# Kernel tuning notes

Hardware: AMD Instinct MI355X
Metric: run time of the kernel (lower is better)

Reference implementation:

```python
import jax, jax.numpy as jnp
import numpy as np
import math

B, T, C_IN = 4, 2048, 1024
HIDDEN, HEADS = 1024, 8
HEAD_DIM = HIDDEN // HEADS
OUT_DIM = 1024
EPS = 1e-8


def setup_inputs() -> dict:
    key = jax.random.key(0)
    ks = jax.random.split(key, 12)
    s_in = 1.0 / math.sqrt(C_IN)
    s_h = 1.0 / math.sqrt(HIDDEN)
    x = jax.random.normal(ks[0], (B, T, C_IN), dtype=jnp.float32)
    # causal keep-mask (True = keep), broadcast over batch
    attn_mask = jnp.broadcast_to(jnp.tril(jnp.ones((T, T), dtype=bool)), (B, T, T))
    Wu = jax.random.normal(ks[1], (HIDDEN, C_IN), dtype=jnp.float32) * s_in
    bu = jnp.zeros((HIDDEN,), dtype=jnp.float32)
    Wv = jax.random.normal(ks[2], (HIDDEN, C_IN), dtype=jnp.float32) * s_in
    bv = jnp.zeros((HIDDEN,), dtype=jnp.float32)
    Wq = jax.random.normal(ks[3], (HIDDEN, C_IN), dtype=jnp.float32) * s_in
    bq = jnp.zeros((HIDDEN,), dtype=jnp.float32)
    Wk = jax.random.normal(ks[4], (HIDDEN, C_IN), dtype=jnp.float32) * s_in
    bk = jnp.zeros((HIDDEN,), dtype=jnp.float32)
    Wf = jax.random.normal(ks[5], (OUT_DIM, HIDDEN), dtype=jnp.float32) * s_h
    bf = jnp.zeros((OUT_DIM,), dtype=jnp.float32)
    g_norm = jnp.ones((HIDDEN,), dtype=jnp.float32)
    return {"x": x, "attn_mask": attn_mask, "Wu": Wu, "bu": bu, "Wv": Wv,
            "bv": bv, "Wq": Wq, "bq": bq, "Wk": Wk, "bk": bk,
            "Wf": Wf, "bf": bf, "g_norm": g_norm}


def _heads(t):  # (B,T,HIDDEN) -> (B,H,T,D)
    b, s, _ = t.shape
    return t.reshape(b, s, HEADS, HEAD_DIM).transpose(0, 2, 1, 3)


def reference(x, attn_mask, Wu, bu, Wv, bv, Wq, bq, Wk, bk, Wf, bf, g_norm):
    silu = jax.nn.silu
    U = silu(x @ Wu.T + bu)
    V = silu(x @ Wv.T + bv)
    Q = silu(x @ Wq.T + bq)
    K = silu(x @ Wk.T + bk)
    Qh, Kh, Vh = _heads(Q), _heads(K), _heads(V)
    scale = 1.0 / math.sqrt(HEAD_DIM)
    logits = jnp.einsum('bhtd,bhsd->bhts', Qh, Kh) * scale
    A = jnp.maximum(silu(logits), 0.0)
    A = jnp.where(attn_mask[:, None, :, :], A, 0.0)
    denom = A.sum(axis=-1, keepdims=True)
    A = jnp.where(denom > 1e-12, A / (denom + EPS), 0.0)
    AVh = jnp.einsum('bhts,bhsd->bhtd', A, Vh)
    AV = AVh.transpose(0, 2, 1, 3).reshape(x.shape[0], x.shape[1], HIDDEN)
    # RMSNorm (torch nn.RMSNorm default eps = dtype eps)
    rms_eps = jnp.finfo(AV.dtype).eps
    AV_norm = AV * jax.lax.rsqrt(jnp.mean(AV * AV, axis=-1, keepdims=True) + rms_eps) * g_norm
    UV = AV_norm * U
    return UV @ Wf.T + bf
```

## Files before the change

kernel.cpp:

```cpp
#include <hip/hip_runtime.h>
#include <hip/hip_bf16.h>
#include <stdint.h>

#define Tlen  2048
#define M_TOK 8192

typedef __attribute__((ext_vector_type(8))) __bf16 bf16x8;
typedef __attribute__((ext_vector_type(4))) float  f32x4;
typedef unsigned short u16;
typedef unsigned int   u32;
typedef unsigned long long u64;

__device__ __forceinline__ float b2f(u16 u) {
  union { float f; u32 i; } v; v.i = ((u32)u) << 16; return v.f;
}
__device__ __forceinline__ u16 f2b(float f) {
  u32 x = __float_as_uint(f);
  return (u16)((x + 0x7FFFu + ((x >> 16) & 1u)) >> 16);
}
__device__ __forceinline__ u32 f2b2(float lo, float hi) {
  __hip_bfloat162 h = __float22bfloat162_rn(float2{lo, hi});
  return *reinterpret_cast<u32*>(&h);
}
__device__ __forceinline__ bf16x8 ld8(const u16* p) {
  return *reinterpret_cast<const bf16x8*>(p);
}
__device__ __forceinline__ bool probe_bf16(const void* g) {
  return *(const u32*)g == 0x3F803F80u;
}
__device__ __forceinline__ void stage8(u16* dst, const void* src, size_t eidx, bool isbf) {
  if (isbf) {
    *(uint4*)dst = *(const uint4*)((const u16*)src + eidx);
  } else {
    const float* f = (const float*)src + eidx;
    float4 a = *(const float4*)f;
    float4 b = *(const float4*)(f + 4);
    u32 t[4] = { f2b2(a.x, a.y), f2b2(a.z, a.w), f2b2(b.x, b.y), f2b2(b.z, b.w) };
    *(uint4*)dst = *(uint4*)t;
  }
}
__device__ __forceinline__ void gl_lds16(const void* g, void* l) {
  __builtin_amdgcn_global_load_lds(
      (const __attribute__((address_space(1))) u32*)g,
      (__attribute__((address_space(3))) u32*)l, 16, 0, 0);
}
__device__ __forceinline__ int swz128(int r, int c) {
  return r * 128 + ((((c >> 3) ^ (r & 15))) << 3) + (c & 7);
}

__global__ __launch_bounds__(256) void prep1(
    const void* __restrict__ x,
    const void* __restrict__ Wu, const void* __restrict__ Wv,
    const void* __restrict__ Wq, const void* __restrict__ Wk,
    const void* __restrict__ bu, const void* __restrict__ bv,
    const void* __restrict__ bq, const void* __restrict__ bk,
    u16* __restrict__ xb, u16* __restrict__ Wcat, u16* __restrict__ bcat,
    const void* __restrict__ gprobe)
{
  const bool isbf = probe_bf16(gprobe);
  long i = (long)blockIdx.x * 256 + threadIdx.x;
  if (i < 1048576) { stage8(&xb[i * 8], x, (size_t)i * 8, isbf); return; }
  i -= 1048576;
  if (i < 524288) {
    int w = (int)(i >> 17); long e = i & 131071;
    const void* s = (w == 0) ? Wu : (w == 1) ? Wv : (w == 2) ? Wq : Wk;
    stage8(&Wcat[((size_t)w << 20) + e * 8], s, (size_t)e * 8, isbf); return;
  }
  i -= 524288;
  if (i < 512) {
    int w = (int)(i >> 7); int e = (int)(i & 127);
    const void* s = (w == 0) ? bu : (w == 1) ? bv : (w == 2) ? bq : bk;
    stage8(&bcat[w * 1024 + e * 8], s, (size_t)e * 8, isbf);
  }
}

__global__ __launch_bounds__(256) void prep2(
    const void* __restrict__ Wf, const void* __restrict__ bf_,
    u16* __restrict__ Wfb, u16* __restrict__ bfb,
    const void* __restrict__ gprobe)
{
  const bool isbf = probe_bf16(gprobe);
  long i = (long)blockIdx.x * 256 + threadIdx.x;
  if (i < 131072) { stage8(&Wfb[i * 8], Wf, (size_t)i * 8, isbf); return; }
  i -= 131072;
  if (i < 128) stage8(&bfb[i * 8], bf_, (size_t)i * 8, isbf);
}

__global__ __launch_bounds__(256) void gemm_proj(
    const u16* __restrict__ X,
    const u16* __restrict__ W,
    const u16* __restrict__ bias,
    u16* __restrict__ U, u16* __restrict__ Vt,
    u16* __restrict__ Qb, u16* __restrict__ Kb)
{
  __shared__ u16 SMEM[16384];
  u16* Xs = SMEM;
  u16* Ws = SMEM + 8192;
  const int tid  = threadIdx.x;
  const int lane = tid & 63;
  const int wave = tid >> 6;
  const int l15  = lane & 15;
  const int quad = lane >> 4;
  const int wr   = wave & 1;
  const int wc   = wave >> 1;
  const int m0 = blockIdx.y * 128;
  const int n0 = blockIdx.x * 128;

  const int ro = lane >> 3;
  const int ch = lane & 7;
  const int cc = ch ^ ro;

  f32x4 acc[4][4] = {};

  for (int k0 = 0; k0 < 1024; k0 += 64) {
    __syncthreads();
#pragma unroll
    for (int j = 0; j < 4; j++) {
      int r0 = wave * 32 + j * 8;
      gl_lds16(X + (size_t)(m0 + r0 + ro) * 1024 + k0 + cc * 8, &Xs[r0 * 64]);
      gl_lds16(W + (size_t)(n0 + r0 + ro) * 1024 + k0 + cc * 8, &Ws[r0 * 64]);
    }
    __syncthreads();

#pragma unroll
    for (int kk = 0; kk < 64; kk += 32) {
      bf16x8 a[4], b[4];
      const int g = (kk >> 3) + quad;
      const int lch = (g ^ (l15 & 7)) << 3;
#pragma unroll
      for (int mt = 0; mt < 4; mt++)
        a[mt] = ld8(&Xs[(wr * 64 + mt * 16 + l15) * 64 + lch]);
#pragma unroll
      for (int nt = 0; nt < 4; nt++)
        b[nt] = ld8(&Ws[(wc * 64 + nt * 16 + l15) * 64 + lch]);
#pragma unroll
      for (int mt = 0; mt < 4; mt++)
#pragma unroll
        for (int nt = 0; nt < 4; nt++)
          acc[mt][nt] = __builtin_amdgcn_mfma_f32_16x16x32_bf16(a[mt], b[nt], acc[mt][nt], 0, 0, 0);
    }
  }

  const int grp = blockIdx.x >> 3;

  if (grp != 1) {
    u16* dst = (grp == 0) ? U : (grp == 2) ? Qb : Kb;
    const float postmul = (grp == 3) ? 0.08838834764831845f : 1.0f;
#pragma unroll
    for (int nt = 0; nt < 4; nt++) {
      int ng = n0 + wc * 64 + nt * 16 + l15;
      float bv = b2f(bias[ng]);
      int ncol = ng & 1023;
#pragma unroll
      for (int mt = 0; mt < 4; mt++) {
#pragma unroll
        for (int r = 0; r < 4; r++) {
          int m = m0 + wr * 64 + mt * 16 + quad * 4 + r;
          float v = acc[mt][nt][r] + bv;
          v = v * __builtin_amdgcn_rcpf(1.0f + __expf(-v));
          dst[(size_t)m * 1024 + ncol] = f2b(v * postmul);
        }
      }
    }
    return;
  }

  u16* Ls = SMEM;
  __syncthreads();
#pragma unroll
  for (int nt = 0; nt < 4; nt++) {
    int ng = n0 + wc * 64 + nt * 16 + l15;
    float bv = b2f(bias[ng]);
    int nl = wc * 64 + nt * 16 + l15;
#pragma unroll
    for (int mt = 0; mt < 4; mt++) {
      float vv[4];
#pragma unroll
      for (int r = 0; r < 4; r++) {
        float v = acc[mt][nt][r] + bv;
        vv[r] = v * __builtin_amdgcn_rcpf(1.0f + __expf(-v));
      }
      int ml = wr * 64 + mt * 16 + quad * 4;
      u64 pk = (u64)f2b2(vv[0], vv[1]) | ((u64)f2b2(vv[2], vv[3]) << 32);
      *(u64*)&Ls[swz128(nl, ml)] = pk;
    }
  }
  __syncthreads();

  const int rr = tid & 127;
  const int c0 = tid >> 7;
  const int bh = (blockIdx.y >> 4) * 8 + (blockIdx.x & 7);
  const int t0 = (blockIdx.y & 15) * 128;
#pragma unroll
  for (int p = 0; p < 8; p++) {
    int chunk = c0 + p * 2;
    uint4 vv = *(const uint4*)&Ls[swz128(rr, chunk * 8)];
    *(uint4*)&Vt[((size_t)bh * 128 + rr) * 2048 + t0 + chunk * 8] = vv;
  }
}

__global__ __launch_bounds__(256) void gemm_final(
    const u16* __restrict__ X,
    const u16* __restrict__ W,
    const u16* __restrict__ bias,
    float* __restrict__ O)
{
  __shared__ u16 Xs[128 * 64];
  __shared__ u16 Ws[64 * 64];
  const int tid  = threadIdx.x;
  const int lane = tid & 63;
  const int wave = tid >> 6;
  const int l15  = lane & 15;
  const int quad = lane >> 4;
  const int m0 = blockIdx.y * 128;
  const int n0 = blockIdx.x * 64;

  const int ro = lane >> 3;
  const int ch = lane & 7;
  const int cc = ch ^ ro;

  f32x4 acc[2][4] = {};

  for (int k0 = 0; k0 < 1024; k0 += 64) {
    __syncthreads();
#pragma unroll
    for (int j = 0; j < 4; j++) {
      int r0 = wave * 32 + j * 8;
      gl_lds16(X + (size_t)(m0 + r0 + ro) * 1024 + k0 + cc * 8, &Xs[r0 * 64]);
    }
#pragma unroll
    for (int j = 0; j < 2; j++) {
      int r0 = wave * 16 + j * 8;
      gl_lds16(W + (size_t)(n0 + r0 + ro) * 1024 + k0 + cc * 8, &Ws[r0 * 64]);
    }
    __syncthreads();

#pragma unroll
    for (int kk = 0; kk < 64; kk += 32) {
      bf16x8 a[2], b[4];
      const int g = (kk >> 3) + quad;
      const int lch = (g ^ (l15 & 7)) << 3;
#pragma unroll
      for (int mt = 0; mt < 2; mt++)
        a[mt] = ld8(&Xs[(wave * 32 + mt * 16 + l15) * 64 + lch]);
#pragma unroll
      for (int nt = 0; nt < 4; nt++)
        b[nt] = ld8(&Ws[(nt * 16 + l15) * 64 + lch]);
#pragma unroll
      for (int mt = 0; mt < 2; mt++)
#pragma unroll
        for (int nt = 0; nt < 4; nt++)
          acc[mt][nt] = __builtin_amdgcn_mfma_f32_16x16x32_bf16(a[mt], b[nt], acc[mt][nt], 0, 0, 0);
    }
  }

#pragma unroll
  for (int nt = 0; nt < 4; nt++) {
    int n = n0 + nt * 16 + l15;
    float bv = b2f(bias[n]);
#pragma unroll
    for (int mt = 0; mt < 2; mt++)
#pragma unroll
      for (int r = 0; r < 4; r++) {
        int m = m0 + wave * 32 + mt * 16 + quad * 4 + r;
        O[(size_t)m * 1024 + n] = acc[mt][nt][r] + bv;
      }
  }
}

__global__ __launch_bounds__(256, 4) void attn_kernel(
    const u16* __restrict__ Q,
    const u16* __restrict__ K,
    const u16* __restrict__ Vt,
    u16* __restrict__ AV)
{
  __shared__ u16 Ks[64 * 128];
  __shared__ u16 Vts[128 * 64];
  u16* As = Ks;

  const int tid  = threadIdx.x;
  const int lane = tid & 63;
  const int wave = tid >> 6;
  const int l15  = lane & 15;
  const int quad = lane >> 4;
  const int qt = 31 - (blockIdx.x >> 5);
  const int bh = blockIdx.x & 31;
  const int q0 = qt * 64;
  const size_t rowbase = (size_t)(bh >> 3) * Tlen;
  const int cbase = (bh & 7) * 128;
  const size_t vbase = (size_t)bh * 128 * 2048;
  const int mrow = wave * 16;

  bf16x8 bq[4];
#pragma unroll
  for (int kk = 0; kk < 4; kk++)
    bq[kk] = ld8(&Q[(rowbase + q0 + mrow + l15) * 1024 + cbase + kk * 32 + quad * 8]);

  f32x4 avacc[8] = {};
  float denom = 0.f;
  const int t_abs = q0 + mrow + l15;

  for (int s0 = 0; s0 <= q0; s0 += 64) {
    __syncthreads();
    {
      const int ro16 = lane >> 4, ch16 = lane & 15;
#pragma unroll
      for (int j = 0; j < 4; j++) {
        int r0 = wave * 16 + j * 4;
        int cc = ch16 ^ ((r0 + ro16) & 15);
        gl_lds16(&K[(rowbase + s0 + r0 + ro16) * 1024 + cbase + cc * 8], &Ks[r0 * 128]);
      }
      const int ro8 = lane >> 3, ch8 = lane & 7;
#pragma unroll
      for (int j = 0; j < 4; j++) {
        int d0 = wave * 32 + j * 8;
        int cc = ch8 ^ ((d0 + ro8) & 7);
        gl_lds16(&Vt[vbase + (size_t)(d0 + ro8) * 2048 + s0 + cc * 8], &Vts[d0 * 64]);
      }
    }
    __syncthreads();

    f32x4 sacc[4] = {};
#pragma unroll
    for (int kk = 0; kk < 4; kk++) {
      bf16x8 a[4];
      const int lch = (((kk * 4) + quad) ^ l15) << 3;
#pragma unroll
      for (int nt = 0; nt < 4; nt++)
        a[nt] = ld8(&Ks[(nt * 16 + l15) * 128 + lch]);
#pragma unroll
      for (int nt = 0; nt < 4; nt++)
        sacc[nt] = __builtin_amdgcn_mfma_f32_16x16x32_bf16(a[nt], bq[kk], sacc[nt], 0, 0, 0);
    }
    __syncthreads();

    const bool maskneed = (s0 + 63 > q0 + mrow);
    float rs = 0.f;
#pragma unroll
    for (int nt = 0; nt < 4; nt++) {
      float aa[4];
#pragma unroll
      for (int r = 0; r < 4; r++) {
        int s_abs = s0 + nt * 16 + quad * 4 + r;
        float z = sacc[nt][r];
        float a = fmaxf(z, 0.f) * __builtin_amdgcn_rcpf(1.0f + __expf(-z));
        if (maskneed && (s_abs > t_abs)) a = 0.0f;
        rs += a;
        aa[r] = a;
      }
      u64 pk = (u64)f2b2(aa[0], aa[1]) | ((u64)f2b2(aa[2], aa[3]) << 32);
      *(u64*)&As[(mrow + l15) * 72 + nt * 16 + quad * 4] = pk;
    }
    rs += __shfl_xor(rs, 16);
    rs += __shfl_xor(rs, 32);
    denom += rs;

#pragma unroll
    for (int kk = 0; kk < 2; kk++) {
      bf16x8 a, b[8];
      const int lch8 = (((kk * 4) + quad) ^ (l15 & 7)) << 3;
      a = ld8(&As[(mrow + l15) * 72 + kk * 32 + quad * 8]);
#pragma unroll
      for (int dt = 0; dt < 8; dt++)
        b[dt] = ld8(&Vts[(dt * 16 + l15) * 64 + lch8]);
#pragma unroll
      for (int dt = 0; dt < 8; dt++)
        avacc[dt] = __builtin_amdgcn_mfma_f32_16x16x32_bf16(a, b[dt], avacc[dt], 0, 0, 0);
    }
  }

  __syncthreads();
  u16* Ls = Ks;
#pragma unroll
  for (int r = 0; r < 4; r++) {
    float dn = __shfl(denom, (lane & 48) | (quad * 4 + r));
    float sc = (dn > 1e-12f) ? __builtin_amdgcn_rcpf(dn + 1e-8f) : 0.0f;
    int rl = mrow + quad * 4 + r;
#pragma unroll
    for (int dt = 0; dt < 8; dt++)
      Ls[swz128(rl, dt * 16 + l15)] = f2b(avacc[dt][r] * sc);
  }
  __syncthreads();

  const int rr = tid & 63;
  const int c0 = tid >> 6;
#pragma unroll
  for (int p = 0; p < 4; p++) {
    int chunk = c0 + p * 4;
    uint4 vv = *(const uint4*)&Ls[swz128(rr, chunk * 8)];
    *(uint4*)&AV[(rowbase + q0 + rr) * 1024 + cbase + chunk * 8] = vv;
  }
}

__global__ __launch_bounds__(256) void rms_mul(
    const u16* __restrict__ AV, const u16* __restrict__ U,
    const void* __restrict__ g, u16* __restrict__ Y)
{
  const bool isbf = probe_bf16(g);
  const int row = blockIdx.x;
  const int tid = threadIdx.x;
  const size_t base = (size_t)row * 1024;
  uint2 pav = *(const uint2*)&AV[base + tid * 4];
  const u16* pe = (const u16*)&pav;
  float v[4];
  float ss = 0.f;
#pragma unroll
  for (int j = 0; j < 4; j++) { v[j] = b2f(pe[j]); ss += v[j] * v[j]; }
#pragma unroll
  for (int m = 1; m < 64; m <<= 1) ss += __shfl_xor(ss, m);
  __shared__ float red[4];
  if ((tid & 63) == 0) red[tid >> 6] = ss;
  __syncthreads();
  float tot = red[0] + red[1] + red[2] + red[3];
  float rinv = rsqrtf(tot * (1.0f / 1024.0f) + 1.1920929e-7f);
  uint2 pu = *(const uint2*)&U[base + tid * 4];
  const u16* ue = (const u16*)&pu;
  u16 out4[4];
#pragma unroll
  for (int j = 0; j < 4; j++) {
    float gj = isbf ? b2f(((const u16*)g)[tid * 4 + j]) : ((const float*)g)[tid * 4 + j];
    out4[j] = f2b(v[j] * rinv * gj * b2f(ue[j]));
  }
  *(uint2*)&Y[base + tid * 4] = *(uint2*)out4;
}

extern "C" void kernel_launch(void* const* d_in, const int* in_sizes, int n_in,
                              void* d_out, int out_size, void* d_ws, size_t ws_size,
                              hipStream_t stream)
{
  (void)in_sizes; (void)out_size; (void)ws_size;
  const int off = (n_in >= 13) ? 0 : -1;
  const void* x   = d_in[0];
  const void* Wu  = d_in[2 + off];
  const void* bu  = d_in[3 + off];
  const void* Wv  = d_in[4 + off];
  const void* bv  = d_in[5 + off];
  const void* Wq  = d_in[6 + off];
  const void* bq  = d_in[7 + off];
  const void* Wk  = d_in[8 + off];
  const void* bk  = d_in[9 + off];
  const void* Wf  = d_in[10 + off];
  const void* bf_ = d_in[11 + off];
  const void* gn  = d_in[12 + off];

  const size_t NELT = (size_t)M_TOK * 1024;
  u16* xb  = (u16*)d_ws;
  u16* U   = xb + NELT;
  u16* Vt  = U  + NELT;
  u16* Qb  = Vt + NELT;
  u16* Kb  = Qb + NELT;
  u16* AVb = Qb;
  u16* Y   = Kb;
  u16* Wfb = xb;
  u16* bfb = xb + (size_t)1024 * 1024;

  u16* Wcat = (u16*)d_out;
  u16* bcat = Wcat + (size_t)4096 * 1024;

  prep1<<<dim3(6146), 256, 0, stream>>>(x, Wu, Wv, Wq, Wk, bu, bv, bq, bk,
                                        xb, Wcat, bcat, gn);

  gemm_proj<<<dim3(32, 64), 256, 0, stream>>>(xb, Wcat, bcat, U, Vt, Qb, Kb);

  prep2<<<dim3(513), 256, 0, stream>>>(Wf, bf_, Wfb, bfb, gn);

  attn_kernel<<<dim3(1024), 256, 0, stream>>>(Qb, Kb, Vt, AVb);
  rms_mul<<<dim3(M_TOK), 256, 0, stream>>>(AVb, U, gn, Y);

  gemm_final<<<dim3(16, 64), 256, 0, stream>>>(Y, Wfb, bfb, (float*)d_out);
}
```

Measured before the change: 357.2 us.

## Rewrite projection GEMM with 256x256 tiles and double-buffered async LDS pipeline

The fused QKVU projection GEMM now uses 512-thread blocks computing 256x256 output tiles with 8 waves. Global-to-LDS loads are double-buffered and interleaved with MFMA groups, and s_setprio raises priority around the MFMA bursts. Block IDs are remapped so neighbouring blocks share operands in cache. The V-transpose epilogue runs in two passes through 128KB of LDS. This aims to raise MFMA utilisation and hide load latency, at the cost of larger LDS use, lower occupancy and fragile hand-counted vmcnt waits.

After: 338.2 us, median of 3. -5.3%, faster.

```diff
diff --git a/kernel.cpp b/kernel.cpp
--- a/kernel.cpp
+++ b/kernel.cpp
@@ -86,77 +86,130 @@
   if (i < 128) stage8(&bfb[i * 8], bf_, (size_t)i * 8, isbf);
 }
 
-__global__ __launch_bounds__(256) void gemm_proj(
+__global__ __launch_bounds__(512, 2) void gemm_proj(
     const u16* __restrict__ X,
     const u16* __restrict__ W,
     const u16* __restrict__ bias,
     u16* __restrict__ U, u16* __restrict__ Vt,
     u16* __restrict__ Qb, u16* __restrict__ Kb)
 {
-  __shared__ u16 SMEM[16384];
-  u16* Xs = SMEM;
-  u16* Ws = SMEM + 8192;
+  __shared__ __align__(16) u16 SMEM[65536];
   const int tid  = threadIdx.x;
   const int lane = tid & 63;
   const int wave = tid >> 6;
+  const int wm   = wave >> 2;
+  const int wn   = wave & 3;
   const int l15  = lane & 15;
   const int quad = lane >> 4;
-  const int wr   = wave & 1;
-  const int wc   = wave >> 1;
-  const int m0 = blockIdx.y * 128;
-  const int n0 = blockIdx.x * 128;
-
-  const int ro = lane >> 3;
-  const int ch = lane & 7;
-  const int cc = ch ^ ro;
-
-  f32x4 acc[4][4] = {};
-
-  for (int k0 = 0; k0 < 1024; k0 += 64) {
-    __syncthreads();
-#pragma unroll
-    for (int j = 0; j < 4; j++) {
-      int r0 = wave * 32 + j * 8;
-      gl_lds16(X + (size_t)(m0 + r0 + ro) * 1024 + k0 + cc * 8, &Xs[r0 * 64]);
-      gl_lds16(W + (size_t)(n0 + r0 + ro) * 1024 + k0 + cc * 8, &Ws[r0 * 64]);
-    }
-    __syncthreads();
-
-#pragma unroll
-    for (int kk = 0; kk < 64; kk += 32) {
-      bf16x8 a[4], b[4];
-      const int g = (kk >> 3) + quad;
-      const int lch = (g ^ (l15 & 7)) << 3;
-#pragma unroll
-      for (int mt = 0; mt < 4; mt++)
-        a[mt] = ld8(&Xs[(wr * 64 + mt * 16 + l15) * 64 + lch]);
-#pragma unroll
-      for (int nt = 0; nt < 4; nt++)
-        b[nt] = ld8(&Ws[(wc * 64 + nt * 16 + l15) * 64 + lch]);
-#pragma unroll
-      for (int mt = 0; mt < 4; mt++)
-#pragma unroll
-        for (int nt = 0; nt < 4; nt++)
-          acc[mt][nt] = __builtin_amdgcn_mfma_f32_16x16x32_bf16(a[mt], b[nt], acc[mt][nt], 0, 0, 0);
-    }
-  }
-
-  const int grp = blockIdx.x >> 3;
+
+  const int id = ((blockIdx.x & 7) << 6) | (blockIdx.x >> 3);
+  const int by = id >> 4;
+  const int bx = id & 15;
+  const int m0 = by << 8;
+  const int n0 = bx << 8;
+
+  const int slotoff = (l15 * 4 + quad) * 8;
+  const u16* Xsrc = X + (size_t)(m0 + wave * 32 + (lane >> 2)) * 1024 + ((lane & 3) << 3);
+  const u16* Wsrc = W + (size_t)(n0 + wave * 32 + (lane >> 2)) * 1024 + ((lane & 3) << 3);
+  const int ldsw = wave << 10;
+
+  bf16x8 a[4], b[4];
+  f32x4 acc[8][4] = {};
+
+#define BAR() __builtin_amdgcn_s_barrier()
+#define WAITV(n) asm volatile("s_waitcnt vmcnt(" #n ")" ::: "memory")
+#define STAGE_A(t, kh, sbuf) do { \
+    const int _kb = ((t) << 6) + ((kh) << 5); \
+    u16* _l = &SMEM[((sbuf) << 14) + ((kh) << 13) + ldsw]; \
+    gl_lds16(Xsrc + _kb, _l); \
+    gl_lds16(Xsrc + 16384 + _kb, _l + 512); \
+  } while (0)
+#define STAGE_B(t, kh, sbuf) do { \
+    const int _kb = ((t) << 6) + ((kh) << 5); \
+    u16* _l = &SMEM[32768 + ((sbuf) << 14) + ((kh) << 13) + ldsw]; \
+    gl_lds16(Wsrc + _kb, _l); \
+    gl_lds16(Wsrc + 16384 + _kb, _l + 512); \
+  } while (0)
+#define LDA(h, kh, sbuf) do { \
+    const u16* _p = &SMEM[((sbuf) << 14) + ((kh) << 13) + ((wm * 8 + (h) * 4) << 9) + slotoff]; \
+    a[0] = ld8(_p); a[1] = ld8(_p + 512); a[2] = ld8(_p + 1024); a[3] = ld8(_p + 1536); \
+  } while (0)
+#define LDB(kh, sbuf) do { \
+    const u16* _p = &SMEM[32768 + ((sbuf) << 14) + ((kh) << 13) + ((wn * 4) << 9) + slotoff]; \
+    b[0] = ld8(_p); b[1] = ld8(_p + 512); b[2] = ld8(_p + 1024); b[3] = ld8(_p + 1536); \
+  } while (0)
+#define MFMA16(h) do { \
+    __builtin_amdgcn_s_setprio(1); \
+    _Pragma("unroll") \
+    for (int _mt = 0; _mt < 4; _mt++) { \
+      _Pragma("unroll") \
+      for (int _nt = 0; _nt < 4; _nt++) \
+        acc[(h) * 4 + _mt][_nt] = __builtin_amdgcn_mfma_f32_16x16x32_bf16( \
+            a[_mt], b[_nt], acc[(h) * 4 + _mt][_nt], 0, 0, 0); \
+    } \
+    __builtin_amdgcn_s_setprio(0); \
+  } while (0)
+
+  STAGE_A(0, 0, 0); STAGE_B(0, 0, 0); STAGE_A(0, 1, 0); STAGE_B(0, 1, 0);
+  WAITV(4);
+  STAGE_A(1, 0, 1); STAGE_B(1, 0, 1); STAGE_A(1, 1, 1);
+  WAITV(6);
+  BAR();
+
+#define GROUP(t, buf) do { \
+    LDA(0, 0, buf); LDB(0, buf); STAGE_B((t) + 1, 1, (buf) ^ 1); \
+    BAR(); MFMA16(0); BAR(); \
+    LDA(1, 0, buf); STAGE_A((t) + 2, 0, buf); \
+    BAR(); MFMA16(1); BAR(); \
+    LDA(0, 1, buf); LDB(1, buf); STAGE_B((t) + 2, 0, buf); \
+    BAR(); MFMA16(0); BAR(); \
+    LDA(1, 1, buf); STAGE_A((t) + 2, 1, buf); \
+    BAR(); MFMA16(1); WAITV(6); BAR(); \
+  } while (0)
+
+#pragma unroll 1
+  for (int u = 0; u < 14; u += 2) {
+    GROUP(u, 0);
+    GROUP(u + 1, 1);
+  }
+  LDA(0, 0, 0); LDB(0, 0); STAGE_B(15, 1, 1);
+  BAR(); MFMA16(0); BAR();
+  LDA(1, 0, 0);
+  BAR(); MFMA16(1); BAR();
+  LDA(0, 1, 0); LDB(1, 0);
+  BAR(); MFMA16(0); BAR();
+  LDA(1, 1, 0);
+  BAR(); MFMA16(1); WAITV(0); BAR();
+  LDA(0, 0, 1); LDB(0, 1); MFMA16(0);
+  LDA(1, 0, 1); MFMA16(1);
+  LDA(0, 1, 1); LDB(1, 1); MFMA16(0);
+  LDA(1, 1, 1); MFMA16(1);
+
+#undef GROUP
+#undef MFMA16
+#undef LDB
+#undef LDA
+#undef STAGE_B
+#undef STAGE_A
+#undef WAITV
+#undef BAR
+
+  const int grp = bx >> 2;
 
   if (grp != 1) {
     u16* dst = (grp == 0) ? U : (grp == 2) ? Qb : Kb;
     const float postmul = (grp == 3) ? 0.08838834764831845f : 1.0f;
 #pragma unroll
     for (int nt = 0; nt < 4; nt++) {
-      int ng = n0 + wc * 64 + nt * 16 + l15;
-      float bv = b2f(bias[ng]);
-      int ncol = ng & 1023;
-#pragma unroll
-      for (int mt = 0; mt < 4; mt++) {
+      const int ng = n0 + wn * 64 + nt * 16 + l15;
+      const float bv = b2f(bias[ng]);
+      const int ncol = ng & 1023;
+#pragma unroll
+      for (int fm = 0; fm < 8; fm++) {
 #pragma unroll
         for (int r = 0; r < 4; r++) {
-          int m = m0 + wr * 64 + mt * 16 + quad * 4 + r;
-          float v = acc[mt][nt][r] + bv;
+          const int m = m0 + wm * 128 + fm * 16 + quad * 4 + r;
+          float v = acc[fm][nt][r] + bv;
           v = v * __builtin_amdgcn_rcpf(1.0f + __expf(-v));
           dst[(size_t)m * 1024 + ncol] = f2b(v * postmul);
         }
@@ -166,36 +219,42 @@
   }
 
   u16* Ls = SMEM;
-  __syncthreads();
-#pragma unroll
-  for (int nt = 0; nt < 4; nt++) {
-    int ng = n0 + wc * 64 + nt * 16 + l15;
-    float bv = b2f(bias[ng]);
-    int nl = wc * 64 + nt * 16 + l15;
-#pragma unroll
-    for (int mt = 0; mt < 4; mt++) {
-      float vv[4];
-#pragma unroll
-      for (int r = 0; r < 4; r++) {
-        float v = acc[mt][nt][r] + bv;
-        vv[r] = v * __builtin_amdgcn_rcpf(1.0f + __expf(-v));
+  const int hb  = (n0 & 1023) >> 7;
+  const int bh0 = (m0 >> 11) * 8;
+  const int t0  = m0 & 2047;
+#pragma unroll
+  for (int pass = 0; pass < 2; pass++) {
+    __syncthreads();
+    if (wm == pass) {
+#pragma unroll
+      for (int nt = 0; nt < 4; nt++) {
+        const int ng = n0 + wn * 64 + nt * 16 + l15;
+        const float bv = b2f(bias[ng]);
+        const int rowl = wn * 64 + nt * 16 + l15;
+#pragma unroll
+        for (int fm = 0; fm < 8; fm++) {
+          float vv[4];
+#pragma unroll
+          for (int r = 0; r < 4; r++) {
+            float v = acc[fm][nt][r] + bv;
+            vv[r] = v * __builtin_amdgcn_rcpf(1.0f + __expf(-v));
+          }
+          const int coll = fm * 16 + quad * 4;
+          u64 pk = (u64)f2b2(vv[0], vv[1]) | ((u64)f2b2(vv[2], vv[3]) << 32);
+          *(u64*)&Ls[swz128(rowl, coll)] = pk;
+        }
       }
-      int ml = wr * 64 + mt * 16 + quad * 4;
-      u64 pk = (u64)f2b2(vv[0], vv[1]) | ((u64)f2b2(vv[2], vv[3]) << 32);
-      *(u64*)&Ls[swz128(nl, ml)] = pk;
-    }
-  }
-  __syncthreads();
-
-  const int rr = tid & 127;
-  const int c0 = tid >> 7;
-  const int bh = (blockIdx.y >> 4) * 8 + (blockIdx.x & 7);
-  const int t0 = (blockIdx.y & 15) * 128;
-#pragma unroll
-  for (int p = 0; p < 8; p++) {
-    int chunk = c0 + p * 2;
-    uint4 vv = *(const uint4*)&Ls[swz128(rr, chunk * 8)];
-    *(uint4*)&Vt[((size_t)bh * 128 + rr) * 2048 + t0 + chunk * 8] = vv;
+    }
+    __syncthreads();
+    const int rr = tid & 255;
+    const int c0 = tid >> 8;
+#pragma unroll
+    for (int p = 0; p < 8; p++) {
+      const int chunk = c0 + p * 2;
+      uint4 vv4 = *(const uint4*)&Ls[swz128(rr, chunk * 8)];
+      *(uint4*)&Vt[((size_t)(bh0 + hb + (rr >> 7)) * 128 + (rr & 127)) * 2048
+                   + t0 + pass * 128 + chunk * 8] = vv4;
+    }
   }
 }
 
@@ -460,7 +519,7 @@
   prep1<<<dim3(6146), 256, 0, stream>>>(x, Wu, Wv, Wq, Wk, bu, bv, bq, bk,
                                         xb, Wcat, bcat, gn);
 
-  gemm_proj<<<dim3(32, 64), 256, 0, stream>>>(xb, Wcat, bcat, U, Vt, Qb, Kb);
+  gemm_proj<<<dim3(512), 512, 0, stream>>>(xb, Wcat, bcat, U, Vt, Qb, Kb);
 
   prep2<<<dim3(513), 256, 0, stream>>>(Wf, bf_, Wfb, bfb, gn);
 
```
